# Kernel optimization log

Hardware: AMD Instinct MI355X
Metric: run time of the kernel (lower is better)

The kernel has to match this reference:

```python
import jax, jax.numpy as jnp
import numpy as np
import math

ETA = 1.0          # self.ddim_sampling_eta
SCALE = 1.0        # self.scale (unused in eval ddim path here)
IOU_THR = 0.5
SCORE_THR = 0.5


def cosine_alphas_cumprod(timesteps=1000, s=0.008):
    steps = timesteps + 1
    x = np.linspace(0, timesteps, steps, dtype=np.float64)
    ac = np.cos((x / timesteps + s) / (1 + s) * math.pi * 0.5) ** 2
    ac = ac / ac[0]
    betas = np.clip(1 - ac[1:] / ac[:-1], 0, 0.999)
    alphas = 1.0 - betas
    return np.cumprod(alphas).astype(np.float32)  # [timesteps]


def setup_inputs() -> dict:
    key = jax.random.key(0)
    ks = jax.random.split(key, 8)
    B, N, C, H = 128, 500, 80, 6
    boxes_t = jax.random.normal(ks[0], (B, N, 2), dtype=jnp.float32)
    predicted_class = jax.random.normal(ks[1], (H, B, N, C), dtype=jnp.float32)
    predicted_boxes = jax.random.uniform(ks[2], (H, B, N, 2), dtype=jnp.float32)
    noise = jax.random.normal(ks[3], (B, N, 2), dtype=jnp.float32)
    fresh_noise = jax.random.normal(ks[4], (B, N, 2), dtype=jnp.float32)
    alphas_cumprod = jnp.asarray(cosine_alphas_cumprod(1000))
    return {
        "boxes_t": boxes_t,
        "predicted_class": predicted_class,
        "predicted_boxes": predicted_boxes,
        "noise": noise,
        "fresh_noise": fresh_noise,
        "alphas_cumprod": alphas_cumprod,
        "t_now": 999,
        "t_next": 499,
    }


def _nms_1d_single(boxes_cw, scores, labels):
    # boxes_cw: [N,2] (center, width) 1-D intervals; class-aware greedy NMS.
    N = boxes_cw.shape[0]
    c = boxes_cw[:, 0]
    w = jnp.maximum(boxes_cw[:, 1], 1e-4)
    x1, x2 = c - w / 2, c + w / 2
    inter = jnp.maximum(0.0, jnp.minimum(x2[:, None], x2[None, :])
                        - jnp.maximum(x1[:, None], x1[None, :]))
    union = w[:, None] + w[None, :] - inter
    iou = inter / jnp.maximum(union, 1e-9)                       # [N,N]
    same = labels[:, None] == labels[None, :]
    order = jnp.argsort(-scores)
    iou_s = iou[order][:, order]
    same_s = same[order][:, order]
    idx = jnp.arange(N)

    def body(i, suppressed):
        keep_i = jnp.logical_not(suppressed[i])
        row = keep_i & (iou_s[i] > IOU_THR) & same_s[i] & (idx > i)
        return suppressed | row

    suppressed = jax.lax.fori_loop(0, N, body, jnp.zeros((N,), bool))
    keep_sorted = jnp.logical_not(suppressed)
    return jnp.zeros((N,), bool).at[order].set(keep_sorted)      # original order


def reference(boxes_t, predicted_class, predicted_boxes, noise, fresh_noise,
              alphas_cumprod, t_now, t_next):
    ac = alphas_cumprod
    boxes_start = predicted_boxes[-1]                            # [B,N,2]

    # predict_noise_from_start (extract -> scalar gather at t_now)
    sqrt_recip = jnp.sqrt(1.0 / ac[t_now])
    sqrt_recipm1 = jnp.sqrt(1.0 / ac[t_now] - 1.0)
    pred_noise = (sqrt_recip * boxes_t - boxes_start) / sqrt_recipm1

    # box renewal: keep mask from sigmoid-max of predicted_class[-1][0]
    score0 = jax.nn.sigmoid(predicted_class[-1][0])              # [N,C]
    keep = jnp.max(score0, axis=-1) > SCORE_THR                  # [N]

    # DDIM step
    alpha, alpha_next = ac[t_now], ac[t_next]
    sigma = ETA * jnp.sqrt((1 - alpha / alpha_next) * (1 - alpha_next) / (1 - alpha))
    cc = jnp.sqrt(1 - alpha_next - sigma ** 2)
    upd = boxes_start * jnp.sqrt(alpha_next) + cc * pred_noise + sigma * noise
    # removed slots are renewed with fresh gaussian proposals (mask form of concat)
    boxes_next = jnp.where(keep[None, :, None], upd, fresh_noise)  # [B,N,2]

    # postprocessing: softmax over classes (drop last bg class), max -> scores/labels
    probs = jax.nn.softmax(predicted_class[-1], axis=-1)[:, :, :-1]  # [B,N,C-1]
    scores = jnp.max(probs, axis=-1)                             # [B,N]
    labels = jnp.argmax(probs, axis=-1)                          # [B,N]
    nms_keep = jax.vmap(_nms_1d_single)(boxes_start, scores, labels)  # [B,N] bool

    return boxes_next, scores, labels, nms_keep
```

## Files before the change

### kernel.cpp

```cpp
#include <hip/hip_runtime.h>
#include <float.h>

#define BB 128
#define NN 500
#define CC 80
#define NH 6
#define NP 512

typedef unsigned long long u64;
typedef unsigned int u32;

__global__ __launch_bounds__(256) void scores_labels_keep_kernel(
    const float* __restrict__ pc,
    float* __restrict__ scores,
    float* __restrict__ labels,
    int* __restrict__ keep) {
    const int rl = threadIdx.x >> 2;
    const int q = threadIdx.x & 3;
    const int row = blockIdx.x * 64 + rl;
    if (row >= BB * NN) return;

    const float4* base = (const float4*)(pc + (size_t)(NH - 1) * BB * NN * CC);
    float4 v[5];
#pragma unroll
    for (int k = 0; k < 5; ++k) v[k] = base[(size_t)row * 20 + q + 4 * k];

    float m = v[0].x;
#pragma unroll
    for (int k = 0; k < 5; ++k) {
        m = fmaxf(m, v[k].x); m = fmaxf(m, v[k].y);
        m = fmaxf(m, v[k].z); m = fmaxf(m, v[k].w);
    }
    m = fmaxf(m, __shfl_xor(m, 1));
    m = fmaxf(m, __shfl_xor(m, 2));

    float s = 0.0f;
#pragma unroll
    for (int k = 0; k < 5; ++k) {
        s += expf(v[k].x - m); s += expf(v[k].y - m);
        s += expf(v[k].z - m); s += expf(v[k].w - m);
    }
    s += __shfl_xor(s, 1);
    s += __shfl_xor(s, 2);

    float bv = -FLT_MAX; int bc = 1000;
#pragma unroll
    for (int k = 0; k < 5; ++k) {
        const float* vf = (const float*)&v[k];
#pragma unroll
        for (int j = 0; j < 4; ++j) {
            int c = (q + 4 * k) * 4 + j;
            float val = vf[j];
            if (c < CC - 1 && (val > bv || (val == bv && c < bc))) { bv = val; bc = c; }
        }
    }
#pragma unroll
    for (int off = 1; off < 4; off <<= 1) {
        float ov = __shfl_xor(bv, off);
        int oc = __shfl_xor(bc, off);
        if (ov > bv || (ov == bv && oc < bc)) { bv = ov; bc = oc; }
    }

    if (q == 0) {
        scores[row] = expf(bv - m) / s;
        labels[row] = (float)bc;
        if (row < NN) keep[row] = (m > 0.0f) ? 1 : 0;
    }
}

__global__ __launch_bounds__(512) void nms_kernel(const float* __restrict__ pb,
                                                  const float* __restrict__ scores,
                                                  const float* __restrict__ labels,
                                                  const float* __restrict__ boxes_t,
                                                  const float* __restrict__ noise,
                                                  const float* __restrict__ fresh,
                                                  const float* __restrict__ ac,
                                                  const int* __restrict__ t_now_p,
                                                  const int* __restrict__ t_next_p,
                                                  const int* __restrict__ keep_ws,
                                                  float* __restrict__ out_boxes,
                                                  float* __restrict__ keep_out) {
    __shared__ float4 scs4[NP / 4];
    __shared__ float4 box4u[NP];
    __shared__ float4 sbox4[NP];
    __shared__ int order[NP];
    __shared__ unsigned char lab8[NP];
    __shared__ short brank_s[NP];
    __shared__ short member[NP];
    __shared__ int hist[CC];
    __shared__ int boff[CC];
    __shared__ unsigned char supp[NP];

    const int b = blockIdx.x;
    const int tid = threadIdx.x;
    float* scs = (float*)scs4;

    const float2* boxes = (const float2*)(pb + (size_t)(NH - 1) * BB * NN * 2) + (size_t)b * NN;
    const float* sc = scores + (size_t)b * NN;
    const float* lb = labels + (size_t)b * NN;

    if (tid < CC) hist[tid] = 0;
    supp[tid] = 0;
    if (tid < NN) {
        float2 cw = boxes[tid];
        float w = fmaxf(cw.y, 0.0001f);
        box4u[tid] = make_float4(cw.x - w * 0.5f, cw.x + w * 0.5f, w,
                                 __int_as_float((int)lb[tid]));
        scs[tid] = sc[tid];

        {
            const size_t i = (size_t)b * NN + tid;
            int tn = t_now_p[0], tx = t_next_p[0];
            float a = ac[tn], an = ac[tx];
            float sqrt_recip = sqrtf(1.0f / a);
            float sqrt_recipm1 = sqrtf(1.0f / a - 1.0f);
            float sigma = sqrtf((1.0f - a / an) * (1.0f - an) / (1.0f - a));
            float ccf = sqrtf(1.0f - an - sigma * sigma);
            float sqan = sqrtf(an);
            const float2 bt = ((const float2*)boxes_t)[i];
            float2 o;
            if (keep_ws[tid]) {
                const float2 nz = ((const float2*)noise)[i];
                float pn0 = (sqrt_recip * bt.x - cw.x) / sqrt_recipm1;
                float pn1 = (sqrt_recip * bt.y - cw.y) / sqrt_recipm1;
                o.x = cw.x * sqan + ccf * pn0 + sigma * nz.x;
                o.y = cw.y * sqan + ccf * pn1 + sigma * nz.y;
            } else {
                o = ((const float2*)fresh)[i];
            }
            ((float2*)out_boxes)[i] = o;
        }
    } else {
        box4u[tid] = make_float4(0.f, 0.f, 0.f, __int_as_float(255));
        scs[tid] = -FLT_MAX;
    }
    __syncthreads();

    {
        float si = scs[tid];
        int r = 0;
        for (int j4 = 0; j4 < NP / 4; ++j4) {
            float4 s4 = scs4[j4];
            int j = j4 * 4;
            r += (s4.x > si) || (s4.x == si && (j + 0) < tid);
            r += (s4.y > si) || (s4.y == si && (j + 1) < tid);
            r += (s4.z > si) || (s4.z == si && (j + 2) < tid);
            r += (s4.w > si) || (s4.w == si && (j + 3) < tid);
        }
        order[r] = tid;
    }
    __syncthreads();

    {
        float4 v = box4u[order[tid]];
        sbox4[tid] = v;
        lab8[tid] = (unsigned char)__float_as_int(v.w);
    }
    __syncthreads();

    if (tid < NN) {
        const u32 myl = lab8[tid];
        int cnt = 0;
        const uint4* l16 = (const uint4*)lab8;
        const int nc = (tid >> 4) + 1;
        for (int cI = 0; cI < nc; ++cI) {
            uint4 c = l16[cI];
            int base = cI * 16;
#pragma unroll
            for (int byi = 0; byi < 4; ++byi) {
                cnt += (base + byi      < tid) && (((c.x >> (8 * byi)) & 0xFF) == myl);
                cnt += (base + 4 + byi  < tid) && (((c.y >> (8 * byi)) & 0xFF) == myl);
                cnt += (base + 8 + byi  < tid) && (((c.z >> (8 * byi)) & 0xFF) == myl);
                cnt += (base + 12 + byi < tid) && (((c.w >> (8 * byi)) & 0xFF) == myl);
            }
        }
        brank_s[tid] = (short)cnt;
        atomicAdd(&hist[myl], 1);
    }
    __syncthreads();

    if (tid < 64) {
        int a = (tid < CC) ? hist[tid] : 0;
        int b2 = (tid < CC - 64) ? hist[64 + tid] : 0;
        int sa = a;
#pragma unroll
        for (int d = 1; d < 64; d <<= 1) {
            int t = __shfl_up(sa, d);
            if ((int)tid >= d) sa += t;
        }
        int totalA = __shfl(sa, 63);
        int sb = b2;
#pragma unroll
        for (int d = 1; d < 64; d <<= 1) {
            int t = __shfl_up(sb, d);
            if ((int)tid >= d) sb += t;
        }
        if (tid < CC) boff[tid] = sa - a;
        if (tid < CC - 64) boff[64 + tid] = sb - b2 + totalA;
    }
    __syncthreads();

    if (tid < NN) member[boff[lab8[tid]] + brank_s[tid]] = (short)tid;
    __syncthreads();

    {
        const int wv = tid >> 6;
        const int lane = tid & 63;
        for (int l = wv; l < CC; l += 8) {
            const int n = hist[l];
            if (n <= 1) continue;
            const int off = boff[l];
            if (n <= 64) {
                const bool valid = lane < n;
                int rq = 0;
                float x1 = 0.f, x2 = 0.f, ww = 0.f;
                if (valid) {
                    rq = member[off + lane];
                    float4 v = sbox4[rq];
                    x1 = v.x; x2 = v.y; ww = v.z;
                }
                bool sup = false;
                for (int p = 0; p < n - 1; ++p) {
                    u64 smask = __ballot(sup);
                    bool pAlive = ((smask >> p) & 1ull) == 0ull;
                    float bx1 = __int_as_float(__builtin_amdgcn_readlane(__float_as_int(x1), p));
                    float bx2 = __int_as_float(__builtin_amdgcn_readlane(__float_as_int(x2), p));
                    float bw  = __int_as_float(__builtin_amdgcn_readlane(__float_as_int(ww), p));
                    float inter = fmaxf(0.0f, fminf(bx2, x2) - fmaxf(bx1, x1));
                    float uni = bw + ww - inter;
                    float iou = inter / fmaxf(uni, 1e-9f);
                    sup = sup || (pAlive && valid && (lane > p) && (iou > 0.5f));
                }
                if (valid && sup) supp[rq] = 1;
            } else {
                if (lane == 0) {
                    for (int p = 0; p < n - 1; ++p) {
                        int rp = member[off + p];
                        if (supp[rp]) continue;
                        float4 bp = sbox4[rp];
                        for (int q2 = p + 1; q2 < n; ++q2) {
                            int rqq = member[off + q2];
                            if (supp[rqq]) continue;
                            float4 bq = sbox4[rqq];
                            float inter = fmaxf(0.0f, fminf(bp.y, bq.y) - fmaxf(bp.x, bq.x));
                            float uni = bp.z + bq.z - inter;
                            float iou = inter / fmaxf(uni, 1e-9f);
                            if (iou > 0.5f) supp[rqq] = 1;
                        }
                    }
                }
            }
        }
    }
    __syncthreads();

    if (tid < NN) {
        keep_out[(size_t)b * NN + order[tid]] = supp[tid] ? 0.0f : 1.0f;
    }
}

extern "C" void kernel_launch(void* const* d_in, const int* in_sizes, int n_in,
                              void* d_out, int out_size, void* d_ws, size_t ws_size,
                              hipStream_t stream) {
    const float* boxes_t = (const float*)d_in[0];
    const float* pc      = (const float*)d_in[1];
    const float* pb      = (const float*)d_in[2];
    const float* noise   = (const float*)d_in[3];
    const float* fresh   = (const float*)d_in[4];
    const float* ac      = (const float*)d_in[5];
    const int*   t_now   = (const int*)d_in[6];
    const int*   t_next  = (const int*)d_in[7];

    float* out_boxes  = (float*)d_out;
    float* out_scores = out_boxes + (size_t)BB * NN * 2;
    float* out_labels = out_scores + (size_t)BB * NN;
    float* out_keep   = out_labels + (size_t)BB * NN;

    int* keep_ws = (int*)d_ws;

    scores_labels_keep_kernel<<<(BB * NN) / 64, 256, 0, stream>>>(
        pc, out_scores, out_labels, keep_ws);
    nms_kernel<<<BB, 512, 0, stream>>>(pb, out_scores, out_labels,
                                       boxes_t, noise, fresh, ac, t_now, t_next,
                                       keep_ws, out_boxes, out_keep);
}
```

Baseline: 214.7 us.

## Fuse softmax/argmax into NMS kernel and drop the global sort

Merges the scores/labels kernel into the per-batch NMS kernel, so each of the 128 blocks computes softmax, max and argmax for its own 500 rows and keeps them in shared memory. It removes the full score-rank sort and permutation, replacing them with a within-class rank that counts same-label elements with higher score. It also recomputes the keep mask from batch 0 inside every block. The risk is lower parallelism: the softmax over about 20MB now runs on only 128 blocks instead of 1000, which may limit memory bandwidth.

```diff
diff --git a/kernel.cpp b/kernel.cpp
--- a/kernel.cpp
+++ b/kernel.cpp
@@ -10,81 +10,24 @@
 typedef unsigned long long u64;
 typedef unsigned int u32;
 
-__global__ __launch_bounds__(256) void scores_labels_keep_kernel(
+__global__ __launch_bounds__(512) void fused_kernel(
+    const float* __restrict__ boxes_t,
     const float* __restrict__ pc,
-    float* __restrict__ scores,
-    float* __restrict__ labels,
-    int* __restrict__ keep) {
-    const int rl = threadIdx.x >> 2;
-    const int q = threadIdx.x & 3;
-    const int row = blockIdx.x * 64 + rl;
-    if (row >= BB * NN) return;
-
-    const float4* base = (const float4*)(pc + (size_t)(NH - 1) * BB * NN * CC);
-    float4 v[5];
-#pragma unroll
-    for (int k = 0; k < 5; ++k) v[k] = base[(size_t)row * 20 + q + 4 * k];
-
-    float m = v[0].x;
-#pragma unroll
-    for (int k = 0; k < 5; ++k) {
-        m = fmaxf(m, v[k].x); m = fmaxf(m, v[k].y);
-        m = fmaxf(m, v[k].z); m = fmaxf(m, v[k].w);
-    }
-    m = fmaxf(m, __shfl_xor(m, 1));
-    m = fmaxf(m, __shfl_xor(m, 2));
-
-    float s = 0.0f;
-#pragma unroll
-    for (int k = 0; k < 5; ++k) {
-        s += expf(v[k].x - m); s += expf(v[k].y - m);
-        s += expf(v[k].z - m); s += expf(v[k].w - m);
-    }
-    s += __shfl_xor(s, 1);
-    s += __shfl_xor(s, 2);
-
-    float bv = -FLT_MAX; int bc = 1000;
-#pragma unroll
-    for (int k = 0; k < 5; ++k) {
-        const float* vf = (const float*)&v[k];
-#pragma unroll
-        for (int j = 0; j < 4; ++j) {
-            int c = (q + 4 * k) * 4 + j;
-            float val = vf[j];
-            if (c < CC - 1 && (val > bv || (val == bv && c < bc))) { bv = val; bc = c; }
-        }
-    }
-#pragma unroll
-    for (int off = 1; off < 4; off <<= 1) {
-        float ov = __shfl_xor(bv, off);
-        int oc = __shfl_xor(bc, off);
-        if (ov > bv || (ov == bv && oc < bc)) { bv = ov; bc = oc; }
-    }
-
-    if (q == 0) {
-        scores[row] = expf(bv - m) / s;
-        labels[row] = (float)bc;
-        if (row < NN) keep[row] = (m > 0.0f) ? 1 : 0;
-    }
-}
-
-__global__ __launch_bounds__(512) void nms_kernel(const float* __restrict__ pb,
-                                                  const float* __restrict__ scores,
-                                                  const float* __restrict__ labels,
-                                                  const float* __restrict__ boxes_t,
-                                                  const float* __restrict__ noise,
-                                                  const float* __restrict__ fresh,
-                                                  const float* __restrict__ ac,
-                                                  const int* __restrict__ t_now_p,
-                                                  const int* __restrict__ t_next_p,
-                                                  const int* __restrict__ keep_ws,
-                                                  float* __restrict__ out_boxes,
-                                                  float* __restrict__ keep_out) {
+    const float* __restrict__ pb,
+    const float* __restrict__ noise,
+    const float* __restrict__ fresh,
+    const float* __restrict__ ac,
+    const int* __restrict__ t_now_p,
+    const int* __restrict__ t_next_p,
+    float* __restrict__ out_boxes,
+    float* __restrict__ out_scores,
+    float* __restrict__ out_labels,
+    float* __restrict__ out_keep) {
+
     __shared__ float4 scs4[NP / 4];
     __shared__ float4 box4u[NP];
-    __shared__ float4 sbox4[NP];
-    __shared__ int order[NP];
     __shared__ unsigned char lab8[NP];
+    __shared__ unsigned char keepb[NP];
     __shared__ short brank_s[NP];
     __shared__ short member[NP];
     __shared__ int hist[CC];
@@ -95,83 +38,130 @@
     const int tid = threadIdx.x;
     float* scs = (float*)scs4;
 
-    const float2* boxes = (const float2*)(pb + (size_t)(NH - 1) * BB * NN * 2) + (size_t)b * NN;
-    const float* sc = scores + (size_t)b * NN;
-    const float* lb = labels + (size_t)b * NN;
+    const int quad = tid >> 2;
+    const int q = tid & 3;
 
     if (tid < CC) hist[tid] = 0;
     supp[tid] = 0;
-    if (tid < NN) {
-        float2 cw = boxes[tid];
+    if (tid >= NN) { scs[tid] = -FLT_MAX; lab8[tid] = 255; }
+
+    const float4* rowbase = (const float4*)(pc + (size_t)(NH - 1) * BB * NN * CC
+                                               + (size_t)b * NN * CC);
+#pragma unroll
+    for (int pass = 0; pass < 4; ++pass) {
+        const int row = pass * 128 + quad;
+        if (row < NN) {
+            float4 v[5];
+#pragma unroll
+            for (int k = 0; k < 5; ++k) v[k] = rowbase[(size_t)row * 20 + q + 4 * k];
+            float m = v[0].x;
+#pragma unroll
+            for (int k = 0; k < 5; ++k) {
+                m = fmaxf(m, v[k].x); m = fmaxf(m, v[k].y);
+                m = fmaxf(m, v[k].z); m = fmaxf(m, v[k].w);
+            }
+            m = fmaxf(m, __shfl_xor(m, 1));
+            m = fmaxf(m, __shfl_xor(m, 2));
+            float s = 0.0f;
+#pragma unroll
+            for (int k = 0; k < 5; ++k) {
+                s += expf(v[k].x - m); s += expf(v[k].y - m);
+                s += expf(v[k].z - m); s += expf(v[k].w - m);
+            }
+            s += __shfl_xor(s, 1);
+            s += __shfl_xor(s, 2);
+            float bv = -FLT_MAX; int bc = 1000;
+#pragma unroll
+            for (int k = 0; k < 5; ++k) {
+                const float* vf = (const float*)&v[k];
+#pragma unroll
+                for (int j = 0; j < 4; ++j) {
+                    int c = (q + 4 * k) * 4 + j;
+                    float val = vf[j];
+                    if (c < CC - 1 && (val > bv || (val == bv && c < bc))) { bv = val; bc = c; }
+                }
+            }
+#pragma unroll
+            for (int off = 1; off < 4; off <<= 1) {
+                float ov = __shfl_xor(bv, off);
+                int oc = __shfl_xor(bc, off);
+                if (ov > bv || (ov == bv && oc < bc)) { bv = ov; bc = oc; }
+            }
+            if (q == 0) {
+                float sval = expf(bv - m) / s;
+                out_scores[(size_t)b * NN + row] = sval;
+                out_labels[(size_t)b * NN + row] = (float)bc;
+                scs[row] = sval;
+                lab8[row] = (unsigned char)bc;
+            }
+        }
+    }
+
+    const float4* row0 = (const float4*)(pc + (size_t)(NH - 1) * BB * NN * CC);
+#pragma unroll
+    for (int pass = 0; pass < 4; ++pass) {
+        const int row = pass * 128 + quad;
+        if (row < NN) {
+            float m = -FLT_MAX;
+#pragma unroll
+            for (int k = 0; k < 5; ++k) {
+                float4 v = row0[(size_t)row * 20 + q + 4 * k];
+                m = fmaxf(m, fmaxf(fmaxf(v.x, v.y), fmaxf(v.z, v.w)));
+            }
+            m = fmaxf(m, __shfl_xor(m, 1));
+            m = fmaxf(m, __shfl_xor(m, 2));
+            if (q == 0) keepb[row] = (m > 0.0f) ? 1 : 0;
+        }
+    }
+
+    float2 cw = make_float2(0.f, 0.f);
+    if (tid < NN) {
+        cw = ((const float2*)(pb + (size_t)(NH - 1) * BB * NN * 2))[(size_t)b * NN + tid];
         float w = fmaxf(cw.y, 0.0001f);
-        box4u[tid] = make_float4(cw.x - w * 0.5f, cw.x + w * 0.5f, w,
-                                 __int_as_float((int)lb[tid]));
-        scs[tid] = sc[tid];
-
-        {
-            const size_t i = (size_t)b * NN + tid;
-            int tn = t_now_p[0], tx = t_next_p[0];
-            float a = ac[tn], an = ac[tx];
-            float sqrt_recip = sqrtf(1.0f / a);
-            float sqrt_recipm1 = sqrtf(1.0f / a - 1.0f);
-            float sigma = sqrtf((1.0f - a / an) * (1.0f - an) / (1.0f - a));
-            float ccf = sqrtf(1.0f - an - sigma * sigma);
-            float sqan = sqrtf(an);
-            const float2 bt = ((const float2*)boxes_t)[i];
-            float2 o;
-            if (keep_ws[tid]) {
-                const float2 nz = ((const float2*)noise)[i];
-                float pn0 = (sqrt_recip * bt.x - cw.x) / sqrt_recipm1;
-                float pn1 = (sqrt_recip * bt.y - cw.y) / sqrt_recipm1;
-                o.x = cw.x * sqan + ccf * pn0 + sigma * nz.x;
-                o.y = cw.y * sqan + ccf * pn1 + sigma * nz.y;
-            } else {
-                o = ((const float2*)fresh)[i];
-            }
-            ((float2*)out_boxes)[i] = o;
-        }
-    } else {
-        box4u[tid] = make_float4(0.f, 0.f, 0.f, __int_as_float(255));
-        scs[tid] = -FLT_MAX;
-    }
-    __syncthreads();
-
-    {
-        float si = scs[tid];
-        int r = 0;
-        for (int j4 = 0; j4 < NP / 4; ++j4) {
-            float4 s4 = scs4[j4];
-            int j = j4 * 4;
-            r += (s4.x > si) || (s4.x == si && (j + 0) < tid);
-            r += (s4.y > si) || (s4.y == si && (j + 1) < tid);
-            r += (s4.z > si) || (s4.z == si && (j + 2) < tid);
-            r += (s4.w > si) || (s4.w == si && (j + 3) < tid);
-        }
-        order[r] = tid;
-    }
-    __syncthreads();
-
-    {
-        float4 v = box4u[order[tid]];
-        sbox4[tid] = v;
-        lab8[tid] = (unsigned char)__float_as_int(v.w);
-    }
-    __syncthreads();
+        box4u[tid] = make_float4(cw.x - w * 0.5f, cw.x + w * 0.5f, w, 0.f);
+    }
+    __syncthreads();
+
+    if (tid < NN) {
+        const size_t i = (size_t)b * NN + tid;
+        int tn = t_now_p[0], tx = t_next_p[0];
+        float a = ac[tn], an = ac[tx];
+        float sqrt_recip = sqrtf(1.0f / a);
+        float sqrt_recipm1 = sqrtf(1.0f / a - 1.0f);
+        float sigma = sqrtf((1.0f - a / an) * (1.0f - an) / (1.0f - a));
+        float ccf = sqrtf(1.0f - an - sigma * sigma);
+        float sqan = sqrtf(an);
+        const float2 bt = ((const float2*)boxes_t)[i];
+        float2 o;
+        if (keepb[tid]) {
+            const float2 nz = ((const float2*)noise)[i];
+            float pn0 = (sqrt_recip * bt.x - cw.x) / sqrt_recipm1;
+            float pn1 = (sqrt_recip * bt.y - cw.y) / sqrt_recipm1;
+            o.x = cw.x * sqan + ccf * pn0 + sigma * nz.x;
+            o.y = cw.y * sqan + ccf * pn1 + sigma * nz.y;
+        } else {
+            o = ((const float2*)fresh)[i];
+        }
+        ((float2*)out_boxes)[i] = o;
+    }
 
     if (tid < NN) {
         const u32 myl = lab8[tid];
+        const float si = scs[tid];
         int cnt = 0;
         const uint4* l16 = (const uint4*)lab8;
-        const int nc = (tid >> 4) + 1;
-        for (int cI = 0; cI < nc; ++cI) {
-            uint4 c = l16[cI];
-            int base = cI * 16;
-#pragma unroll
-            for (int byi = 0; byi < 4; ++byi) {
-                cnt += (base + byi      < tid) && (((c.x >> (8 * byi)) & 0xFF) == myl);
-                cnt += (base + 4 + byi  < tid) && (((c.y >> (8 * byi)) & 0xFF) == myl);
-                cnt += (base + 8 + byi  < tid) && (((c.z >> (8 * byi)) & 0xFF) == myl);
-                cnt += (base + 12 + byi < tid) && (((c.w >> (8 * byi)) & 0xFF) == myl);
+        for (int c = 0; c < NP / 16; ++c) {
+            uint4 lv = l16[c];
+            const u32 lw[4] = {lv.x, lv.y, lv.z, lv.w};
+            int base = c * 16;
+#pragma unroll
+            for (int g = 0; g < 4; ++g) {
+                float4 s4 = scs4[c * 4 + g];
+                int j0 = base + 4 * g;
+                cnt += (((lw[g]      ) & 0xFFu) == myl) && ((s4.x > si) || (s4.x == si && (j0 + 0) < tid));
+                cnt += (((lw[g] >>  8) & 0xFFu) == myl) && ((s4.y > si) || (s4.y == si && (j0 + 1) < tid));
+                cnt += (((lw[g] >> 16) & 0xFFu) == myl) && ((s4.z > si) || (s4.z == si && (j0 + 2) < tid));
+                cnt += (((lw[g] >> 24)        ) == myl) && ((s4.w > si) || (s4.w == si && (j0 + 3) < tid));
             }
         }
         brank_s[tid] = (short)cnt;
@@ -216,7 +206,7 @@
                 float x1 = 0.f, x2 = 0.f, ww = 0.f;
                 if (valid) {
                     rq = member[off + lane];
-                    float4 v = sbox4[rq];
+                    float4 v = box4u[rq];
                     x1 = v.x; x2 = v.y; ww = v.z;
                 }
                 bool sup = false;
@@ -237,11 +227,11 @@
                     for (int p = 0; p < n - 1; ++p) {
                         int rp = member[off + p];
                         if (supp[rp]) continue;
-                        float4 bp = sbox4[rp];
+                        float4 bp = box4u[rp];
                         for (int q2 = p + 1; q2 < n; ++q2) {
                             int rqq = member[off + q2];
                             if (supp[rqq]) continue;
-                            float4 bq = sbox4[rqq];
+                            float4 bq = box4u[rqq];
                             float inter = fmaxf(0.0f, fminf(bp.y, bq.y) - fmaxf(bp.x, bq.x));
                             float uni = bp.z + bq.z - inter;
                             float iou = inter / fmaxf(uni, 1e-9f);
@@ -255,7 +245,7 @@
     __syncthreads();
 
     if (tid < NN) {
-        keep_out[(size_t)b * NN + order[tid]] = supp[tid] ? 0.0f : 1.0f;
+        out_keep[(size_t)b * NN + tid] = supp[tid] ? 0.0f : 1.0f;
     }
 }
 
@@ -276,11 +266,7 @@
     float* out_labels = out_scores + (size_t)BB * NN;
     float* out_keep   = out_labels + (size_t)BB * NN;
 
-    int* keep_ws = (int*)d_ws;
-
-    scores_labels_keep_kernel<<<(BB * NN) / 64, 256, 0, stream>>>(
-        pc, out_scores, out_labels, keep_ws);
-    nms_kernel<<<BB, 512, 0, stream>>>(pb, out_scores, out_labels,
-                                       boxes_t, noise, fresh, ac, t_now, t_next,
-                                       keep_ws, out_boxes, out_keep);
+    fused_kernel<<<BB, 512, 0, stream>>>(boxes_t, pc, pb, noise, fresh, ac,
+                                         t_now, t_next,
+                                         out_boxes, out_scores, out_labels, out_keep);
 }
```

New measurement: 219.2 us. 1.02x slower.

## Replace global score sort with per-class bucketing and in-wave score ranking

Applied to the files above, without the earlier changes.

Drops the block-wide O(N^2) score ranking and the reordering passes. Boxes are now bucketed by label with atomic slot allocation, and sorting by score happens only within each class. For small classes the sort is a wave-level readlane rank plus ds_permute, and large classes use a serial selection loop. This cuts shared memory and barriers, but the serial fallback is O(n^2) per class and the atomic placement makes bucket order nondeterministic.

```diff
diff --git a/kernel.cpp b/kernel.cpp
--- a/kernel.cpp
+++ b/kernel.cpp
@@ -80,20 +80,14 @@
                                                   const int* __restrict__ keep_ws,
                                                   float* __restrict__ out_boxes,
                                                   float* __restrict__ keep_out) {
-    __shared__ float4 scs4[NP / 4];
     __shared__ float4 box4u[NP];
-    __shared__ float4 sbox4[NP];
-    __shared__ int order[NP];
-    __shared__ unsigned char lab8[NP];
-    __shared__ short brank_s[NP];
     __shared__ short member[NP];
     __shared__ int hist[CC];
-    __shared__ int boff[CC];
+    __shared__ int cur[CC];
     __shared__ unsigned char supp[NP];
 
     const int b = blockIdx.x;
     const int tid = threadIdx.x;
-    float* scs = (float*)scs4;
 
     const float2* boxes = (const float2*)(pb + (size_t)(NH - 1) * BB * NN * 2) + (size_t)b * NN;
     const float* sc = scores + (size_t)b * NN;
@@ -101,82 +95,37 @@
 
     if (tid < CC) hist[tid] = 0;
     supp[tid] = 0;
+    int myl = -1;
     if (tid < NN) {
         float2 cw = boxes[tid];
         float w = fmaxf(cw.y, 0.0001f);
-        box4u[tid] = make_float4(cw.x - w * 0.5f, cw.x + w * 0.5f, w,
-                                 __int_as_float((int)lb[tid]));
-        scs[tid] = sc[tid];
-
-        {
-            const size_t i = (size_t)b * NN + tid;
-            int tn = t_now_p[0], tx = t_next_p[0];
-            float a = ac[tn], an = ac[tx];
-            float sqrt_recip = sqrtf(1.0f / a);
-            float sqrt_recipm1 = sqrtf(1.0f / a - 1.0f);
-            float sigma = sqrtf((1.0f - a / an) * (1.0f - an) / (1.0f - a));
-            float ccf = sqrtf(1.0f - an - sigma * sigma);
-            float sqan = sqrtf(an);
-            const float2 bt = ((const float2*)boxes_t)[i];
-            float2 o;
-            if (keep_ws[tid]) {
-                const float2 nz = ((const float2*)noise)[i];
-                float pn0 = (sqrt_recip * bt.x - cw.x) / sqrt_recipm1;
-                float pn1 = (sqrt_recip * bt.y - cw.y) / sqrt_recipm1;
-                o.x = cw.x * sqan + ccf * pn0 + sigma * nz.x;
-                o.y = cw.y * sqan + ccf * pn1 + sigma * nz.y;
-            } else {
-                o = ((const float2*)fresh)[i];
-            }
-            ((float2*)out_boxes)[i] = o;
-        }
-    } else {
-        box4u[tid] = make_float4(0.f, 0.f, 0.f, __int_as_float(255));
-        scs[tid] = -FLT_MAX;
-    }
-    __syncthreads();
-
-    {
-        float si = scs[tid];
-        int r = 0;
-        for (int j4 = 0; j4 < NP / 4; ++j4) {
-            float4 s4 = scs4[j4];
-            int j = j4 * 4;
-            r += (s4.x > si) || (s4.x == si && (j + 0) < tid);
-            r += (s4.y > si) || (s4.y == si && (j + 1) < tid);
-            r += (s4.z > si) || (s4.z == si && (j + 2) < tid);
-            r += (s4.w > si) || (s4.w == si && (j + 3) < tid);
-        }
-        order[r] = tid;
-    }
-    __syncthreads();
-
-    {
-        float4 v = box4u[order[tid]];
-        sbox4[tid] = v;
-        lab8[tid] = (unsigned char)__float_as_int(v.w);
-    }
-    __syncthreads();
-
-    if (tid < NN) {
-        const u32 myl = lab8[tid];
-        int cnt = 0;
-        const uint4* l16 = (const uint4*)lab8;
-        const int nc = (tid >> 4) + 1;
-        for (int cI = 0; cI < nc; ++cI) {
-            uint4 c = l16[cI];
-            int base = cI * 16;
-#pragma unroll
-            for (int byi = 0; byi < 4; ++byi) {
-                cnt += (base + byi      < tid) && (((c.x >> (8 * byi)) & 0xFF) == myl);
-                cnt += (base + 4 + byi  < tid) && (((c.y >> (8 * byi)) & 0xFF) == myl);
-                cnt += (base + 8 + byi  < tid) && (((c.z >> (8 * byi)) & 0xFF) == myl);
-                cnt += (base + 12 + byi < tid) && (((c.w >> (8 * byi)) & 0xFF) == myl);
-            }
-        }
-        brank_s[tid] = (short)cnt;
-        atomicAdd(&hist[myl], 1);
-    }
+        myl = (int)lb[tid];
+        box4u[tid] = make_float4(cw.x - w * 0.5f, cw.x + w * 0.5f, w, sc[tid]);
+
+        const size_t i = (size_t)b * NN + tid;
+        int tn = t_now_p[0], tx = t_next_p[0];
+        float a = ac[tn], an = ac[tx];
+        float sqrt_recip = sqrtf(1.0f / a);
+        float sqrt_recipm1 = sqrtf(1.0f / a - 1.0f);
+        float sigma = sqrtf((1.0f - a / an) * (1.0f - an) / (1.0f - a));
+        float ccf = sqrtf(1.0f - an - sigma * sigma);
+        float sqan = sqrtf(an);
+        const float2 bt = ((const float2*)boxes_t)[i];
+        float2 o;
+        if (keep_ws[tid]) {
+            const float2 nz = ((const float2*)noise)[i];
+            float pn0 = (sqrt_recip * bt.x - cw.x) / sqrt_recipm1;
+            float pn1 = (sqrt_recip * bt.y - cw.y) / sqrt_recipm1;
+            o.x = cw.x * sqan + ccf * pn0 + sigma * nz.x;
+            o.y = cw.y * sqan + ccf * pn1 + sigma * nz.y;
+        } else {
+            o = ((const float2*)fresh)[i];
+        }
+        ((float2*)out_boxes)[i] = o;
+    }
+    __syncthreads();
+
+    if (tid < NN) atomicAdd(&hist[myl], 1);
     __syncthreads();
 
     if (tid < 64) {
@@ -195,12 +144,15 @@
             int t = __shfl_up(sb, d);
             if ((int)tid >= d) sb += t;
         }
-        if (tid < CC) boff[tid] = sa - a;
-        if (tid < CC - 64) boff[64 + tid] = sb - b2 + totalA;
-    }
-    __syncthreads();
-
-    if (tid < NN) member[boff[lab8[tid]] + brank_s[tid]] = (short)tid;
+        if (tid < CC) cur[tid] = sa - a;
+        if (tid < CC - 64) cur[64 + tid] = sb - b2 + totalA;
+    }
+    __syncthreads();
+
+    if (tid < NN) {
+        int pos = atomicAdd(&cur[myl], 1);
+        member[pos] = (short)tid;
+    }
     __syncthreads();
 
     {
@@ -209,20 +161,28 @@
         for (int l = wv; l < CC; l += 8) {
             const int n = hist[l];
             if (n <= 1) continue;
-            const int off = boff[l];
+            const int off = cur[l] - n;
             if (n <= 64) {
                 const bool valid = lane < n;
-                int rq = 0;
-                float x1 = 0.f, x2 = 0.f, ww = 0.f;
-                if (valid) {
-                    rq = member[off + lane];
-                    float4 v = sbox4[rq];
-                    x1 = v.x; x2 = v.y; ww = v.z;
+                int id = valid ? (int)member[off + lane] : 0;
+                float4 v = box4u[id];
+                float sco = valid ? v.w : -FLT_MAX;
+                int idk = valid ? id : 0x7FFFFFFF;
+                int r = 0;
+                for (int p = 0; p < n; ++p) {
+                    float sp = __int_as_float(__builtin_amdgcn_readlane(__float_as_int(sco), p));
+                    int ip = __builtin_amdgcn_readlane(idk, p);
+                    r += (sp > sco) || (sp == sco && ip < idk);
                 }
+                int tgt = (valid ? r : lane) << 2;
+                float x1 = __int_as_float(__builtin_amdgcn_ds_permute(tgt, __float_as_int(v.x)));
+                float x2 = __int_as_float(__builtin_amdgcn_ds_permute(tgt, __float_as_int(v.y)));
+                float ww = __int_as_float(__builtin_amdgcn_ds_permute(tgt, __float_as_int(v.z)));
+                int rid  = __builtin_amdgcn_ds_permute(tgt, id);
                 bool sup = false;
                 for (int p = 0; p < n - 1; ++p) {
-                    u64 smask = __ballot(sup);
-                    bool pAlive = ((smask >> p) & 1ull) == 0ull;
+                    u64 alive = __ballot(sup);
+                    bool pAlive = ((alive >> p) & 1ull) == 0ull;
                     float bx1 = __int_as_float(__builtin_amdgcn_readlane(__float_as_int(x1), p));
                     float bx2 = __int_as_float(__builtin_amdgcn_readlane(__float_as_int(x2), p));
                     float bw  = __int_as_float(__builtin_amdgcn_readlane(__float_as_int(ww), p));
@@ -231,21 +191,30 @@
                     float iou = inter / fmaxf(uni, 1e-9f);
                     sup = sup || (pAlive && valid && (lane > p) && (iou > 0.5f));
                 }
-                if (valid && sup) supp[rq] = 1;
+                if (valid && sup) supp[rid] = 1;
             } else {
                 if (lane == 0) {
-                    for (int p = 0; p < n - 1; ++p) {
-                        int rp = member[off + p];
-                        if (supp[rp]) continue;
-                        float4 bp = sbox4[rp];
-                        for (int q2 = p + 1; q2 < n; ++q2) {
-                            int rqq = member[off + q2];
-                            if (supp[rqq]) continue;
-                            float4 bq = sbox4[rqq];
-                            float inter = fmaxf(0.0f, fminf(bp.y, bq.y) - fmaxf(bp.x, bq.x));
-                            float uni = bp.z + bq.z - inter;
-                            float iou = inter / fmaxf(uni, 1e-9f);
-                            if (iou > 0.5f) supp[rqq] = 1;
+                    for (int step = 0; step < n; ++step) {
+                        int bi = -1, bid = 0x7FFFFFFF; float bs = -FLT_MAX;
+                        for (int k = 0; k < n; ++k) {
+                            int id2 = member[off + k];
+                            if (id2 < 0) continue;
+                            float s2 = box4u[id2].w;
+                            if (s2 > bs || (s2 == bs && id2 < bid)) { bs = s2; bid = id2; bi = k; }
+                        }
+                        if (bi < 0) break;
+                        member[off + bi] = -1;
+                        if (!supp[bid]) {
+                            float4 bp = box4u[bid];
+                            for (int k = 0; k < n; ++k) {
+                                int id2 = member[off + k];
+                                if (id2 < 0) continue;
+                                float4 bq = box4u[id2];
+                                float inter = fmaxf(0.0f, fminf(bp.y, bq.y) - fmaxf(bp.x, bq.x));
+                                float uni = bp.z + bq.z - inter;
+                                float iou = inter / fmaxf(uni, 1e-9f);
+                                if (iou > 0.5f) supp[id2] = 1;
+                            }
                         }
                     }
                 }
@@ -255,7 +224,7 @@
     __syncthreads();
 
     if (tid < NN) {
-        keep_out[(size_t)b * NN + order[tid]] = supp[tid] ? 0.0f : 1.0f;
+        keep_out[(size_t)b * NN + tid] = supp[tid] ? 0.0f : 1.0f;
     }
 }
 
```

Result: faster. 192.8 us (-10.2%).
